# Kernel tuning notes

Hardware: AMD Instinct MI355X
Metric: run time of the kernel (lower is better)

## Reference

```python
import jax, jax.numpy as jnp
import numpy as np

SEQ, D_IN, D_OUT = 8192, 768, 768

def setup_inputs() -> dict:
    key = jax.random.key(0)
    k1, k2, k3, k4 = jax.random.split(key, 4)
    scale = 1.0 / np.sqrt(D_IN)
    return {
        "x": jax.random.normal(k1, (SEQ, D_IN), dtype=jnp.float32),
        "w_q": jax.random.normal(k2, (D_OUT, D_IN), dtype=jnp.float32) * scale,
        "w_k": jax.random.normal(k3, (D_OUT, D_IN), dtype=jnp.float32) * scale,
        "w_v": jax.random.normal(k4, (D_OUT, D_IN), dtype=jnp.float32) * scale,
    }

def reference(x, w_q, w_k, w_v):
    # torch Linear: y = x @ W.T (no bias since qkv_bias=False)
    q = x @ w_q.T  # [S, D]
    k = x @ w_k.T  # [S, D]
    v = x @ w_v.T  # [S, D]
    scores = (q @ k.T) / jnp.sqrt(jnp.asarray(k.shape[-1], x.dtype))  # [S, S]
    attn = jax.nn.softmax(scores, axis=-1)
    return attn @ v  # [S, D]
```

## Files before the change

### kernel.cpp

```cpp
#include <hip/hip_runtime.h>

#define SEQ 8192
#define DIM 768

typedef __attribute__((ext_vector_type(8))) short s16x8;
typedef __attribute__((ext_vector_type(4))) float f32x4;

__device__ __forceinline__ unsigned short f2bf(float f) {
  union { float f; unsigned u; } v; v.f = f;
  unsigned r = v.u + 0x7FFFu + ((v.u >> 16) & 1u);
  return (unsigned short)(r >> 16);
}

__device__ __forceinline__ float bf2f(unsigned short s) {
  union { unsigned u; float f; } v; v.u = ((unsigned)s) << 16;
  return v.f;
}

__device__ __forceinline__ void gll16(const void* gsrc, void* ldst) {
  __builtin_amdgcn_global_load_lds(
      (__attribute__((address_space(1))) unsigned int*)gsrc,
      (__attribute__((address_space(3))) unsigned int*)ldst, 16, 0, 0);
}

#define XN4 (SEQ * DIM / 4)
#define WN4 (DIM * DIM / 4)

__global__ void cast_all_kernel(const float* __restrict__ x, const float* __restrict__ wq,
                                const float* __restrict__ wk, const float* __restrict__ wv,
                                unsigned short* __restrict__ dx, unsigned short* __restrict__ dq,
                                unsigned short* __restrict__ dk, unsigned short* __restrict__ dv) {
  int i = blockIdx.x * blockDim.x + threadIdx.x;
  const float* s;
  unsigned short* d;
  int off;
  if (i < XN4) {
    s = x; d = dx; off = i;
  } else {
    int j = i - XN4;
    int wi = j / WN4;
    off = j - wi * WN4;
    s = (wi == 0) ? wq : ((wi == 1) ? wk : wv);
    d = (wi == 0) ? dq : ((wi == 1) ? dk : dv);
  }
  float4 v = ((const float4*)s)[off];
  ushort4 r; r.x = f2bf(v.x); r.y = f2bf(v.y); r.z = f2bf(v.z); r.w = f2bf(v.w);
  ((ushort4*)d)[off] = r;
}

__global__ __launch_bounds__(256, 2)
void proj_kernel(const unsigned short* __restrict__ X,
                 const unsigned short* __restrict__ Wq,
                 const unsigned short* __restrict__ Wk,
                 const unsigned short* __restrict__ Wv,
                 unsigned short* __restrict__ Qb,
                 unsigned short* __restrict__ Kb,
                 unsigned short* __restrict__ Vtb) {
  __shared__ __align__(16) char lds[65536];
  const int tid = threadIdx.x;
  const int lane = tid & 63, wv = tid >> 6;
  const int l15 = lane & 15, l4 = lane >> 4;
  const int mt = blockIdx.x, nt = blockIdx.y, z = blockIdx.z;
  const unsigned short* W = (z == 0) ? Wq : ((z == 1) ? Wk : Wv);

  f32x4 acc[4][4];
#pragma unroll
  for (int i = 0; i < 4; ++i)
#pragma unroll
    for (int j = 0; j < 4; ++j) acc[i][j] = f32x4{0.f, 0.f, 0.f, 0.f};

  auto stage = [&](int kk) {
    char* At = lds + (kk & 1) * 32768;
    char* Bt = At + 16384;
    const int d0 = kk * 64;
#pragma unroll
    for (int i = 0; i < 4; ++i) {
      int s = i * 256 + tid;
      int row = s >> 3, c = (s & 7) ^ (row & 7);
      gll16(X + (long)(mt * 128 + row) * DIM + d0 + c * 8, At + i * 4096 + (wv << 10));
      gll16(W + (long)(nt * 128 + row) * DIM + d0 + c * 8, Bt + i * 4096 + (wv << 10));
    }
  };

  stage(0);
#pragma unroll 1
  for (int kk = 0; kk < 12; ++kk) {
    __syncthreads();
    if (kk + 1 < 12) stage(kk + 1);
    const char* At = lds + (kk & 1) * 32768;
    const char* Bt = At + 16384;
#pragma unroll
    for (int ks = 0; ks < 2; ++ks) {
      const int c = ks * 4 + l4;
      s16x8 a[4], b[4];
#pragma unroll
      for (int mi = 0; mi < 4; ++mi) {
        int row = (wv & 1) * 64 + mi * 16 + l15;
        a[mi] = *(const s16x8*)(At + row * 128 + ((c ^ (row & 7)) << 4));
      }
#pragma unroll
      for (int ni = 0; ni < 4; ++ni) {
        int row = (wv >> 1) * 64 + ni * 16 + l15;
        b[ni] = *(const s16x8*)(Bt + row * 128 + ((c ^ (row & 7)) << 4));
      }
#pragma unroll
      for (int mi = 0; mi < 4; ++mi)
#pragma unroll
        for (int ni = 0; ni < 4; ++ni)
          acc[mi][ni] = __builtin_amdgcn_mfma_f32_16x16x32_bf16(a[mi], b[ni], acc[mi][ni], 0, 0, 0);
    }
  }

#pragma unroll
  for (int mi = 0; mi < 4; ++mi)
#pragma unroll
    for (int ni = 0; ni < 4; ++ni) {
      int row0 = mt * 128 + (wv & 1) * 64 + mi * 16 + l4 * 4;
      int col = nt * 128 + (wv >> 1) * 64 + ni * 16 + l15;
      if (z == 2) {
        ushort4 r;
        r.x = f2bf(acc[mi][ni][0]); r.y = f2bf(acc[mi][ni][1]);
        r.z = f2bf(acc[mi][ni][2]); r.w = f2bf(acc[mi][ni][3]);
        *(ushort4*)(Vtb + (long)(row0 >> 5) * (DIM * 32) + col * 32 + (row0 & 31)) = r;
      } else {
        unsigned short* dst = (z == 0) ? Qb : Kb;
#pragma unroll
        for (int g = 0; g < 4; ++g)
          dst[(long)(row0 + g) * DIM + col] = f2bf(acc[mi][ni][g]);
      }
    }
}

#define SCALE_LOG2E 0.05205878f

__global__ __launch_bounds__(512, 2)
void flash_kernel(const unsigned short* __restrict__ Q,
                  const unsigned short* __restrict__ K,
                  const unsigned short* __restrict__ V,
                  unsigned short* __restrict__ partp,
                  float* __restrict__ outf,
                  float* __restrict__ lout,
                  int kv_len, int norm_out) {
  __shared__ __align__(16) char lds[131072];
  char* Pl = lds + 98304;
  float* l_part = (float*)lds;

  const int tid = threadIdx.x;
  const int lane = tid & 63, wv = tid >> 6;
  const int l15 = lane & 15, l4 = lane >> 4;
  const int qtile = blockIdx.x, split = blockIdx.y;
  const long kv0 = (long)split * kv_len;
  const long qrow0 = (long)qtile * 64;
  const int R = wv & 1;
  const int C = wv >> 1;

  f32x4 acc_o[4][6];
  float acc_lp[8];
#pragma unroll
  for (int i = 0; i < 4; ++i)
#pragma unroll
    for (int j = 0; j < 6; ++j) acc_o[i][j] = f32x4{0.f, 0.f, 0.f, 0.f};
#pragma unroll
  for (int i = 0; i < 8; ++i) acc_lp[i] = 0.f;

  const int niter = kv_len >> 8;

  auto vchunk = [&](int par, int j) -> char* {
    int base = par ? ((j < 5) ? 40960 + j * 8192 : 90112)
                   : ((j < 5) ? j * 8192 : 81920);
    return lds + base;
  };

  auto stageQK = [&](int r, long kbase) {
    char* Qc = lds + (r & 1) * 40960;
    char* Kc = Qc + 8192;
    const int d0 = r * 64;
    {
      int s = tid;
      int row = s >> 3, c = (s & 7) ^ (row & 7);
      gll16(Q + (qrow0 + row) * DIM + d0 + c * 8, Qc + (wv << 10));
    }
#pragma unroll
    for (int i = 0; i < 4; ++i) {
      int s = i * 512 + tid;
      int row = s >> 3, c = (s & 7) ^ (row & 7);
      gll16(K + (kbase + row) * DIM + d0 + c * 8, Kc + i * 8192 + (wv << 10));
    }
  };

  auto stagePV = [&](int v, long kblk0) {
    const int par = v & 1;
    const long blkbase = (kblk0 + v) * (long)(DIM * 32);
    int s = wv * 64 + lane;
    int rp = s >> 3, p3 = s & 7;
    int orig = p3 ^ (rp & 7);
    int vr_in = rp * 2 + (orig >> 2);
    int k4 = orig & 3;
#pragma unroll
    for (int i = 0; i < 6; ++i)
      gll16(V + blkbase + (long)(i * 128 + vr_in) * 32 + k4 * 8, vchunk(par, i) + (wv << 10));
  };

  stageQK(0, kv0);
#pragma unroll 1
  for (int it = 0; it < niter; ++it) {
    const long kb = kv0 + (long)it * 256;
    const long kblk0 = kb >> 5;

    f32x4 acc_s[2][4];
#pragma unroll
    for (int a = 0; a < 2; ++a)
#pragma unroll
      for (int b = 0; b < 4; ++b) acc_s[a][b] = f32x4{0.f, 0.f, 0.f, 0.f};

#pragma unroll 1
    for (int r = 0; r < 12; ++r) {
      __syncthreads();
      if (r + 1 < 12) stageQK(r + 1, kb);
      else stagePV(0, kblk0);
      const char* Qc = lds + (r & 1) * 40960;
      const char* Kc = Qc + 8192;
#pragma unroll
      for (int ks = 0; ks < 2; ++ks) {
        const int c = ks * 4 + l4;
        s16x8 af[2], bk[4];
#pragma unroll
        for (int rt = 0; rt < 2; ++rt) {
          int row = R * 32 + rt * 16 + l15;
          af[rt] = *(const s16x8*)(Qc + row * 128 + ((c ^ (row & 7)) << 4));
        }
#pragma unroll
        for (int ct = 0; ct < 4; ++ct) {
          int kr = C * 64 + ct * 16 + l15;
          bk[ct] = *(const s16x8*)(Kc + kr * 128 + ((c ^ (kr & 7)) << 4));
        }
#pragma unroll
        for (int rt = 0; rt < 2; ++rt)
#pragma unroll
          for (int ct = 0; ct < 4; ++ct)
            acc_s[rt][ct] = __builtin_amdgcn_mfma_f32_16x16x32_bf16(af[rt], bk[ct], acc_s[rt][ct], 0, 0, 0);
      }
    }

#pragma unroll
    for (int rt = 0; rt < 2; ++rt)
#pragma unroll
      for (int ct = 0; ct < 4; ++ct)
#pragma unroll
        for (int g = 0; g < 4; ++g) {
          float p = exp2f(acc_s[rt][ct][g] * SCALE_LOG2E);
          acc_lp[rt * 4 + g] += p;
          int row = R * 32 + rt * 16 + l4 * 4 + g;
          int col = C * 64 + ct * 16 + l15;
          int off = row * 512 + ((((col >> 3) ^ (row & 7))) << 4) + ((col & 7) << 1);
          *(unsigned short*)(Pl + off) = f2bf(p);
        }

#pragma unroll 1
    for (int v = 0; v < 8; ++v) {
      __syncthreads();
      if (v + 1 < 8) stagePV(v + 1, kblk0);
      else if (it + 1 < niter) stageQK(0, kb + 256);
      const int par = v & 1;
      s16x8 pa[4];
      const int ck = v * 4 + l4;
#pragma unroll
      for (int rs = 0; rs < 4; ++rs) {
        int row = rs * 16 + l15;
        int pc = (ck & ~7) | ((ck & 7) ^ (row & 7));
        pa[rs] = *(const s16x8*)(Pl + row * 512 + (pc << 4));
      }
      const int vr_l = wv * 16 + l15;
      const int rp = vr_l >> 1;
      const int p3 = (((l15 & 1) << 2) | l4) ^ (rp & 7);
#pragma unroll
      for (int cc = 0; cc < 3; ++cc)
#pragma unroll
        for (int t = 0; t < 2; ++t) {
          const char* vcb = vchunk(par, cc * 2 + t);
          s16x8 vb = *(const s16x8*)(vcb + rp * 128 + (p3 << 4));
#pragma unroll
          for (int rs = 0; rs < 4; ++rs)
            acc_o[rs][cc * 2 + t] =
                __builtin_amdgcn_mfma_f32_16x16x32_bf16(pa[rs], vb, acc_o[rs][cc * 2 + t], 0, 0, 0);
        }
    }
  }

#pragma unroll
  for (int i = 0; i < 8; ++i) {
    float v = acc_lp[i];
    v += __shfl_xor(v, 1); v += __shfl_xor(v, 2);
    v += __shfl_xor(v, 4); v += __shfl_xor(v, 8);
    acc_lp[i] = v;
  }
  __syncthreads();
  if (l15 == 0) {
#pragma unroll
    for (int rt = 0; rt < 2; ++rt)
#pragma unroll
      for (int g = 0; g < 4; ++g)
        l_part[C * 64 + R * 32 + rt * 16 + l4 * 4 + g] = acc_lp[rt * 4 + g];
  }
  __syncthreads();

  if (!norm_out) {
    if (tid < 64)
      lout[(long)split * SEQ + qrow0 + tid] =
          l_part[tid] + l_part[64 + tid] + l_part[128 + tid] + l_part[192 + tid];
#pragma unroll
    for (int rt = 0; rt < 4; ++rt) {
      int row = rt * 16 + l4 * 4;
#pragma unroll
      for (int j = 0; j < 6; ++j) {
        int cc = j >> 1, t = j & 1;
        int col = (cc * 16 + wv + 8 * t) * 16 + l15;
#pragma unroll
        for (int g = 0; g < 4; ++g)
          partp[(long)split * SEQ * DIM + (qrow0 + row + g) * DIM + col] = f2bf(acc_o[rt][j][g]);
      }
    }
  } else {
    float linv[4][4];
#pragma unroll
    for (int rt = 0; rt < 4; ++rt)
#pragma unroll
      for (int g = 0; g < 4; ++g) {
        int row = rt * 16 + l4 * 4 + g;
        linv[rt][g] = 1.0f / (l_part[row] + l_part[64 + row] + l_part[128 + row] + l_part[192 + row]);
      }
#pragma unroll
    for (int rt = 0; rt < 4; ++rt) {
      int row = rt * 16 + l4 * 4;
#pragma unroll
      for (int j = 0; j < 6; ++j) {
        int cc = j >> 1, t = j & 1;
        int col = (cc * 16 + wv + 8 * t) * 16 + l15;
#pragma unroll
        for (int g = 0; g < 4; ++g)
          outf[(qrow0 + row + g) * DIM + col] = acc_o[rt][j][g] * linv[rt][g];
      }
    }
  }
}

__global__ void combine_kernel(const unsigned short* __restrict__ part,
                               const float* __restrict__ lsum,
                               float* __restrict__ out, int n4) {
  int i = blockIdx.x * blockDim.x + threadIdx.x;
  if (i >= n4) return;
  int row = (i * 4) / DIM;
  ushort4 p0 = ((const ushort4*)part)[i];
  ushort4 p1 = ((const ushort4*)(part + (long)SEQ * DIM))[i];
  float inv = 1.0f / (lsum[row] + lsum[SEQ + row]);
  float4 o;
  o.x = (bf2f(p0.x) + bf2f(p1.x)) * inv;
  o.y = (bf2f(p0.y) + bf2f(p1.y)) * inv;
  o.z = (bf2f(p0.z) + bf2f(p1.z)) * inv;
  o.w = (bf2f(p0.w) + bf2f(p1.w)) * inv;
  ((float4*)out)[i] = o;
}

extern "C" void kernel_launch(void* const* d_in, const int* in_sizes, int n_in,
                              void* d_out, int out_size, void* d_ws, size_t ws_size,
                              hipStream_t stream) {
  const float* x = (const float*)d_in[0];
  const float* wq = (const float*)d_in[1];
  const float* wk = (const float*)d_in[2];
  const float* wv = (const float*)d_in[3];
  float* out = (float*)d_out;
  char* ws = (char*)d_ws;

  const size_t o_xbf = 0;
  const size_t o_wq = o_xbf + (size_t)SEQ * DIM * 2;
  const size_t o_wk = o_wq + (size_t)DIM * DIM * 2;
  const size_t o_wv = o_wk + (size_t)DIM * DIM * 2;
  const size_t o_q = o_wv + (size_t)DIM * DIM * 2;
  const size_t o_k = o_q + (size_t)SEQ * DIM * 2;
  const size_t o_vt = o_k + (size_t)SEQ * DIM * 2;
  const size_t o_part = o_vt + (size_t)SEQ * DIM * 2;
  const size_t o_l = o_part + (size_t)2 * SEQ * DIM * 2;
  const size_t total_g2 = o_l + (size_t)2 * SEQ * 4;

  unsigned short* Xbf = (unsigned short*)(ws + o_xbf);
  unsigned short* Wqb = (unsigned short*)(ws + o_wq);
  unsigned short* Wkb = (unsigned short*)(ws + o_wk);
  unsigned short* Wvb = (unsigned short*)(ws + o_wv);
  unsigned short* Qb = (unsigned short*)(ws + o_q);
  unsigned short* Kb = (unsigned short*)(ws + o_k);
  unsigned short* Vtb = (unsigned short*)(ws + o_vt);
  unsigned short* part = (unsigned short*)(ws + o_part);
  float* lbuf = (float*)(ws + o_l);

  const int G = (ws_size >= total_g2) ? 2 : 1;

  cast_all_kernel<<<7872, 256, 0, stream>>>(x, wq, wk, wv, Xbf, Wqb, Wkb, Wvb);
  proj_kernel<<<dim3(64, 6, 3), 256, 0, stream>>>(Xbf, Wqb, Wkb, Wvb, Qb, Kb, Vtb);
  if (G == 2) {
    flash_kernel<<<dim3(128, 2), 512, 0, stream>>>(Qb, Kb, Vtb, part, nullptr, lbuf, SEQ / 2, 0);
    combine_kernel<<<6144, 256, 0, stream>>>(part, lbuf, out, SEQ * DIM / 4);
  } else {
    flash_kernel<<<dim3(128, 1), 512, 0, stream>>>(Qb, Kb, Vtb, nullptr, out, nullptr, SEQ, 1);
  }
}
```

Measured before the change: 316.4 us.

## Shrink flash kernel LDS staging and split KV four ways

The flash kernel's LDS staging is halved: Q/K chunks now cover 32 columns instead of 64 over 24 steps, and each V block is staged in two half-D pieces over 16 steps. The footprint drops from 128KB to 80KB, with a new 4-way XOR swizzle for 64-byte rows. The launcher now prefers a 4-way KV split when the workspace allows, and the combine kernel takes a generic split count. The aim is more resident blocks and more grid parallelism, at the cost of twice as many barriers and smaller per-step MFMA batches.

After: 399.6 us. 1.26x slower.

```diff
diff --git a/kernel.cpp b/kernel.cpp
--- a/kernel.cpp
+++ b/kernel.cpp
@@ -141,8 +141,8 @@
                   float* __restrict__ outf,
                   float* __restrict__ lout,
                   int kv_len, int norm_out) {
-  __shared__ __align__(16) char lds[131072];
-  char* Pl = lds + 98304;
+  __shared__ __align__(16) char lds[81920];
+  char* Pl = lds + 49152;
   float* l_part = (float*)lds;
 
   const int tid = threadIdx.x;
@@ -165,40 +165,36 @@
 
   const int niter = kv_len >> 8;
 
-  auto vchunk = [&](int par, int j) -> char* {
-    int base = par ? ((j < 5) ? 40960 + j * 8192 : 90112)
-                   : ((j < 5) ? j * 8192 : 81920);
-    return lds + base;
+  auto stageQK = [&](int r, long kbase) {
+    char* buf = lds + (r & 1) * 24576;
+    char* Qc = buf;
+    char* Kc = buf + 4096;
+    const int d0 = r * 32;
+    if (tid < 256) {
+      int row = tid >> 2, p = tid & 3;
+      int c = p ^ ((row >> 1) & 3);
+      gll16(Q + (qrow0 + row) * DIM + d0 + c * 8, Qc + (wv << 10));
+    }
+#pragma unroll
+    for (int i = 0; i < 2; ++i) {
+      int s = i * 512 + tid;
+      int row = s >> 2, p = s & 3;
+      int c = p ^ ((row >> 1) & 3);
+      gll16(K + (kbase + row) * DIM + d0 + c * 8, Kc + i * 8192 + (wv << 10));
+    }
   };
 
-  auto stageQK = [&](int r, long kbase) {
-    char* Qc = lds + (r & 1) * 40960;
-    char* Kc = Qc + 8192;
-    const int d0 = r * 64;
-    {
-      int s = tid;
-      int row = s >> 3, c = (s & 7) ^ (row & 7);
-      gll16(Q + (qrow0 + row) * DIM + d0 + c * 8, Qc + (wv << 10));
-    }
-#pragma unroll
-    for (int i = 0; i < 4; ++i) {
+  auto stagePV = [&](int v, long kblk0) {
+    char* Vc = lds + (v & 1) * 24576;
+    const long blkbase = (kblk0 + (v >> 1)) * (long)(DIM * 32);
+    const int dh = v & 1;
+#pragma unroll
+    for (int i = 0; i < 3; ++i) {
       int s = i * 512 + tid;
-      int row = s >> 3, c = (s & 7) ^ (row & 7);
-      gll16(K + (kbase + row) * DIM + d0 + c * 8, Kc + i * 8192 + (wv << 10));
-    }
-  };
-
-  auto stagePV = [&](int v, long kblk0) {
-    const int par = v & 1;
-    const long blkbase = (kblk0 + v) * (long)(DIM * 32);
-    int s = wv * 64 + lane;
-    int rp = s >> 3, p3 = s & 7;
-    int orig = p3 ^ (rp & 7);
-    int vr_in = rp * 2 + (orig >> 2);
-    int k4 = orig & 3;
-#pragma unroll
-    for (int i = 0; i < 6; ++i)
-      gll16(V + blkbase + (long)(i * 128 + vr_in) * 32 + k4 * 8, vchunk(par, i) + (wv << 10));
+      int vr = s >> 2, p = s & 3;
+      int c = p ^ ((vr >> 1) & 3);
+      gll16(V + blkbase + (long)(dh * 384 + vr) * 32 + c * 8, Vc + i * 8192 + (wv << 10));
+    }
   };
 
   stageQK(0, kv0);
@@ -214,32 +210,29 @@
       for (int b = 0; b < 4; ++b) acc_s[a][b] = f32x4{0.f, 0.f, 0.f, 0.f};
 
 #pragma unroll 1
-    for (int r = 0; r < 12; ++r) {
+    for (int r = 0; r < 24; ++r) {
       __syncthreads();
-      if (r + 1 < 12) stageQK(r + 1, kb);
+      if (r + 1 < 24) stageQK(r + 1, kb);
       else stagePV(0, kblk0);
-      const char* Qc = lds + (r & 1) * 40960;
-      const char* Kc = Qc + 8192;
-#pragma unroll
-      for (int ks = 0; ks < 2; ++ks) {
-        const int c = ks * 4 + l4;
-        s16x8 af[2], bk[4];
-#pragma unroll
-        for (int rt = 0; rt < 2; ++rt) {
-          int row = R * 32 + rt * 16 + l15;
-          af[rt] = *(const s16x8*)(Qc + row * 128 + ((c ^ (row & 7)) << 4));
-        }
-#pragma unroll
-        for (int ct = 0; ct < 4; ++ct) {
-          int kr = C * 64 + ct * 16 + l15;
-          bk[ct] = *(const s16x8*)(Kc + kr * 128 + ((c ^ (kr & 7)) << 4));
-        }
-#pragma unroll
-        for (int rt = 0; rt < 2; ++rt)
-#pragma unroll
-          for (int ct = 0; ct < 4; ++ct)
-            acc_s[rt][ct] = __builtin_amdgcn_mfma_f32_16x16x32_bf16(af[rt], bk[ct], acc_s[rt][ct], 0, 0, 0);
-      }
+      const char* buf = lds + (r & 1) * 24576;
+      const char* Qc = buf;
+      const char* Kc = buf + 4096;
+      s16x8 af[2], bk[4];
+#pragma unroll
+      for (int rt = 0; rt < 2; ++rt) {
+        int row = R * 32 + rt * 16 + l15;
+        af[rt] = *(const s16x8*)(Qc + row * 64 + ((l4 ^ ((row >> 1) & 3)) << 4));
+      }
+#pragma unroll
+      for (int ct = 0; ct < 4; ++ct) {
+        int kr = C * 64 + ct * 16 + l15;
+        bk[ct] = *(const s16x8*)(Kc + kr * 64 + ((l4 ^ ((kr >> 1) & 3)) << 4));
+      }
+#pragma unroll
+      for (int rt = 0; rt < 2; ++rt)
+#pragma unroll
+        for (int ct = 0; ct < 4; ++ct)
+          acc_s[rt][ct] = __builtin_amdgcn_mfma_f32_16x16x32_bf16(af[rt], bk[ct], acc_s[rt][ct], 0, 0, 0);
     }
 
 #pragma unroll
@@ -256,34 +249,32 @@
           *(unsigned short*)(Pl + off) = f2bf(p);
         }
 
-#pragma unroll 1
-    for (int v = 0; v < 8; ++v) {
+    s16x8 pa[4];
+#pragma unroll 2
+    for (int v = 0; v < 16; ++v) {
       __syncthreads();
-      if (v + 1 < 8) stagePV(v + 1, kblk0);
+      if (v + 1 < 16) stagePV(v + 1, kblk0);
       else if (it + 1 < niter) stageQK(0, kb + 256);
-      const int par = v & 1;
-      s16x8 pa[4];
-      const int ck = v * 4 + l4;
-#pragma unroll
-      for (int rs = 0; rs < 4; ++rs) {
-        int row = rs * 16 + l15;
-        int pc = (ck & ~7) | ((ck & 7) ^ (row & 7));
-        pa[rs] = *(const s16x8*)(Pl + row * 512 + (pc << 4));
-      }
-      const int vr_l = wv * 16 + l15;
-      const int rp = vr_l >> 1;
-      const int p3 = (((l15 & 1) << 2) | l4) ^ (rp & 7);
-#pragma unroll
-      for (int cc = 0; cc < 3; ++cc)
-#pragma unroll
-        for (int t = 0; t < 2; ++t) {
-          const char* vcb = vchunk(par, cc * 2 + t);
-          s16x8 vb = *(const s16x8*)(vcb + rp * 128 + (p3 << 4));
-#pragma unroll
-          for (int rs = 0; rs < 4; ++rs)
-            acc_o[rs][cc * 2 + t] =
-                __builtin_amdgcn_mfma_f32_16x16x32_bf16(pa[rs], vb, acc_o[rs][cc * 2 + t], 0, 0, 0);
+      const char* Vc = lds + (v & 1) * 24576;
+      const int dh = v & 1;
+      if (dh == 0) {
+        const int ck = (v >> 1) * 4 + l4;
+#pragma unroll
+        for (int rs = 0; rs < 4; ++rs) {
+          int row = rs * 16 + l15;
+          int pc = (ck & ~7) | ((ck & 7) ^ (row & 7));
+          pa[rs] = *(const s16x8*)(Pl + row * 512 + (pc << 4));
         }
+      }
+#pragma unroll
+      for (int j = 0; j < 3; ++j) {
+        int vr = j * 128 + wv * 16 + l15;
+        s16x8 vb = *(const s16x8*)(Vc + vr * 64 + ((l4 ^ ((vr >> 1) & 3)) << 4));
+#pragma unroll
+        for (int rs = 0; rs < 4; ++rs)
+          acc_o[rs][dh * 3 + j] =
+              __builtin_amdgcn_mfma_f32_16x16x32_bf16(pa[rs], vb, acc_o[rs][dh * 3 + j], 0, 0, 0);
+      }
     }
   }
 
@@ -346,18 +337,20 @@
 
 __global__ void combine_kernel(const unsigned short* __restrict__ part,
                                const float* __restrict__ lsum,
-                               float* __restrict__ out, int n4) {
+                               float* __restrict__ out, int n4, int nsplit) {
   int i = blockIdx.x * blockDim.x + threadIdx.x;
   if (i >= n4) return;
   int row = (i * 4) / DIM;
-  ushort4 p0 = ((const ushort4*)part)[i];
-  ushort4 p1 = ((const ushort4*)(part + (long)SEQ * DIM))[i];
-  float inv = 1.0f / (lsum[row] + lsum[SEQ + row]);
-  float4 o;
-  o.x = (bf2f(p0.x) + bf2f(p1.x)) * inv;
-  o.y = (bf2f(p0.y) + bf2f(p1.y)) * inv;
-  o.z = (bf2f(p0.z) + bf2f(p1.z)) * inv;
-  o.w = (bf2f(p0.w) + bf2f(p1.w)) * inv;
+  float4 o = {0.f, 0.f, 0.f, 0.f};
+  float l = 0.f;
+#pragma unroll 4
+  for (int g = 0; g < nsplit; ++g) {
+    ushort4 p = ((const ushort4*)(part + (long)g * SEQ * DIM))[i];
+    o.x += bf2f(p.x); o.y += bf2f(p.y); o.z += bf2f(p.z); o.w += bf2f(p.w);
+    l += lsum[(long)g * SEQ + row];
+  }
+  float inv = 1.0f / l;
+  o.x *= inv; o.y *= inv; o.z *= inv; o.w *= inv;
   ((float4*)out)[i] = o;
 }
 
@@ -379,8 +372,10 @@
   const size_t o_k = o_q + (size_t)SEQ * DIM * 2;
   const size_t o_vt = o_k + (size_t)SEQ * DIM * 2;
   const size_t o_part = o_vt + (size_t)SEQ * DIM * 2;
-  const size_t o_l = o_part + (size_t)2 * SEQ * DIM * 2;
-  const size_t total_g2 = o_l + (size_t)2 * SEQ * 4;
+  const size_t o_l4 = o_part + (size_t)4 * SEQ * DIM * 2;
+  const size_t total_g4 = o_l4 + (size_t)4 * SEQ * 4;
+  const size_t o_l2 = o_part + (size_t)2 * SEQ * DIM * 2;
+  const size_t total_g2 = o_l2 + (size_t)2 * SEQ * 4;
 
   unsigned short* Xbf = (unsigned short*)(ws + o_xbf);
   unsigned short* Wqb = (unsigned short*)(ws + o_wq);
@@ -390,15 +385,19 @@
   unsigned short* Kb = (unsigned short*)(ws + o_k);
   unsigned short* Vtb = (unsigned short*)(ws + o_vt);
   unsigned short* part = (unsigned short*)(ws + o_part);
+
+  int G;
+  size_t o_l;
+  if (ws_size >= total_g4) { G = 4; o_l = o_l4; }
+  else if (ws_size >= total_g2) { G = 2; o_l = o_l2; }
+  else { G = 1; o_l = o_part; }
   float* lbuf = (float*)(ws + o_l);
-
-  const int G = (ws_size >= total_g2) ? 2 : 1;
 
   cast_all_kernel<<<7872, 256, 0, stream>>>(x, wq, wk, wv, Xbf, Wqb, Wkb, Wvb);
   proj_kernel<<<dim3(64, 6, 3), 256, 0, stream>>>(Xbf, Wqb, Wkb, Wvb, Qb, Kb, Vtb);
-  if (G == 2) {
-    flash_kernel<<<dim3(128, 2), 512, 0, stream>>>(Qb, Kb, Vtb, part, nullptr, lbuf, SEQ / 2, 0);
-    combine_kernel<<<6144, 256, 0, stream>>>(part, lbuf, out, SEQ * DIM / 4);
+  if (G > 1) {
+    flash_kernel<<<dim3(128, G), 512, 0, stream>>>(Qb, Kb, Vtb, part, nullptr, lbuf, SEQ / G, 0);
+    combine_kernel<<<6144, 256, 0, stream>>>(part, lbuf, out, SEQ * DIM / 4, G);
   } else {
     flash_kernel<<<dim3(128, 1), 512, 0, stream>>>(Qb, Kb, Vtb, nullptr, out, nullptr, SEQ, 1);
   }
```

## Split key range four ways, prefetch P fragments, and raise MFMA wave priority

Applied to the files above, without the earlier changes.

Splits the key dimension into up to four partitions when the workspace is large enough, launching 512 flash blocks instead of 256 and generalising the combine kernel to sum any number of partial outputs. The PV loop is unrolled with double-buffered P fragments so the LDS reads for the next chunk are issued while the current chunk's MFMAs run. s_setprio is raised around the MFMA sequences. The extra split adds partial-output writes and combine traffic, and fixed work per block is amortised over fewer keys.

New measurement: 465.2 us. 47.0% more time.

```diff
diff --git a/kernel.cpp b/kernel.cpp
--- a/kernel.cpp
+++ b/kernel.cpp
@@ -234,11 +234,13 @@
           int kr = C * 64 + ct * 16 + l15;
           bk[ct] = *(const s16x8*)(Kc + kr * 128 + ((c ^ (kr & 7)) << 4));
         }
+        __builtin_amdgcn_s_setprio(1);
 #pragma unroll
         for (int rt = 0; rt < 2; ++rt)
 #pragma unroll
           for (int ct = 0; ct < 4; ++ct)
             acc_s[rt][ct] = __builtin_amdgcn_mfma_f32_16x16x32_bf16(af[rt], bk[ct], acc_s[rt][ct], 0, 0, 0);
+        __builtin_amdgcn_s_setprio(0);
       }
     }
 
@@ -256,20 +258,22 @@
           *(unsigned short*)(Pl + off) = f2bf(p);
         }
 
-#pragma unroll 1
-    for (int v = 0; v < 8; ++v) {
+    s16x8 paA[4], paB[4];
+    auto ldp = [&](s16x8 (&pp)[4], int v) {
+      const int ck = v * 4 + l4;
+#pragma unroll
+      for (int rs = 0; rs < 4; ++rs) {
+        int row = rs * 16 + l15;
+        int pc = (ck & ~7) | ((ck & 7) ^ (row & 7));
+        pp[rs] = *(const s16x8*)(Pl + row * 512 + (pc << 4));
+      }
+    };
+    auto pvchunk = [&](s16x8 (&pa)[4], s16x8 (&pn)[4], int v, bool first) {
       __syncthreads();
       if (v + 1 < 8) stagePV(v + 1, kblk0);
       else if (it + 1 < niter) stageQK(0, kb + 256);
+      if (first) ldp(pa, 0);
       const int par = v & 1;
-      s16x8 pa[4];
-      const int ck = v * 4 + l4;
-#pragma unroll
-      for (int rs = 0; rs < 4; ++rs) {
-        int row = rs * 16 + l15;
-        int pc = (ck & ~7) | ((ck & 7) ^ (row & 7));
-        pa[rs] = *(const s16x8*)(Pl + row * 512 + (pc << 4));
-      }
       const int vr_l = wv * 16 + l15;
       const int rp = vr_l >> 1;
       const int p3 = (((l15 & 1) << 2) | l4) ^ (rp & 7);
@@ -279,12 +283,23 @@
         for (int t = 0; t < 2; ++t) {
           const char* vcb = vchunk(par, cc * 2 + t);
           s16x8 vb = *(const s16x8*)(vcb + rp * 128 + (p3 << 4));
+          __builtin_amdgcn_s_setprio(1);
 #pragma unroll
           for (int rs = 0; rs < 4; ++rs)
             acc_o[rs][cc * 2 + t] =
                 __builtin_amdgcn_mfma_f32_16x16x32_bf16(pa[rs], vb, acc_o[rs][cc * 2 + t], 0, 0, 0);
+          __builtin_amdgcn_s_setprio(0);
         }
-    }
+      if (v + 1 < 8) ldp(pn, v + 1);
+    };
+    pvchunk(paA, paB, 0, true);
+    pvchunk(paB, paA, 1, false);
+    pvchunk(paA, paB, 2, false);
+    pvchunk(paB, paA, 3, false);
+    pvchunk(paA, paB, 4, false);
+    pvchunk(paB, paA, 5, false);
+    pvchunk(paA, paB, 6, false);
+    pvchunk(paB, paA, 7, false);
   }
 
 #pragma unroll
@@ -346,18 +361,20 @@
 
 __global__ void combine_kernel(const unsigned short* __restrict__ part,
                                const float* __restrict__ lsum,
-                               float* __restrict__ out, int n4) {
+                               float* __restrict__ out, int n4, int nsplit) {
   int i = blockIdx.x * blockDim.x + threadIdx.x;
   if (i >= n4) return;
   int row = (i * 4) / DIM;
-  ushort4 p0 = ((const ushort4*)part)[i];
-  ushort4 p1 = ((const ushort4*)(part + (long)SEQ * DIM))[i];
-  float inv = 1.0f / (lsum[row] + lsum[SEQ + row]);
-  float4 o;
-  o.x = (bf2f(p0.x) + bf2f(p1.x)) * inv;
-  o.y = (bf2f(p0.y) + bf2f(p1.y)) * inv;
-  o.z = (bf2f(p0.z) + bf2f(p1.z)) * inv;
-  o.w = (bf2f(p0.w) + bf2f(p1.w)) * inv;
+  float4 o = {0.f, 0.f, 0.f, 0.f};
+  float l = 0.f;
+#pragma unroll 4
+  for (int g = 0; g < nsplit; ++g) {
+    ushort4 p = ((const ushort4*)(part + (long)g * SEQ * DIM))[i];
+    o.x += bf2f(p.x); o.y += bf2f(p.y); o.z += bf2f(p.z); o.w += bf2f(p.w);
+    l += lsum[(long)g * SEQ + row];
+  }
+  float inv = 1.0f / l;
+  o.x *= inv; o.y *= inv; o.z *= inv; o.w *= inv;
   ((float4*)out)[i] = o;
 }
 
@@ -379,8 +396,10 @@
   const size_t o_k = o_q + (size_t)SEQ * DIM * 2;
   const size_t o_vt = o_k + (size_t)SEQ * DIM * 2;
   const size_t o_part = o_vt + (size_t)SEQ * DIM * 2;
-  const size_t o_l = o_part + (size_t)2 * SEQ * DIM * 2;
-  const size_t total_g2 = o_l + (size_t)2 * SEQ * 4;
+  const size_t o_l4 = o_part + (size_t)4 * SEQ * DIM * 2;
+  const size_t total_g4 = o_l4 + (size_t)4 * SEQ * 4;
+  const size_t o_l2 = o_part + (size_t)2 * SEQ * DIM * 2;
+  const size_t total_g2 = o_l2 + (size_t)2 * SEQ * 4;
 
   unsigned short* Xbf = (unsigned short*)(ws + o_xbf);
   unsigned short* Wqb = (unsigned short*)(ws + o_wq);
@@ -390,15 +409,19 @@
   unsigned short* Kb = (unsigned short*)(ws + o_k);
   unsigned short* Vtb = (unsigned short*)(ws + o_vt);
   unsigned short* part = (unsigned short*)(ws + o_part);
+
+  int G;
+  size_t o_l;
+  if (ws_size >= total_g4) { G = 4; o_l = o_l4; }
+  else if (ws_size >= total_g2) { G = 2; o_l = o_l2; }
+  else { G = 1; o_l = o_part; }
   float* lbuf = (float*)(ws + o_l);
-
-  const int G = (ws_size >= total_g2) ? 2 : 1;
 
   cast_all_kernel<<<7872, 256, 0, stream>>>(x, wq, wk, wv, Xbf, Wqb, Wkb, Wvb);
   proj_kernel<<<dim3(64, 6, 3), 256, 0, stream>>>(Xbf, Wqb, Wkb, Wvb, Qb, Kb, Vtb);
-  if (G == 2) {
-    flash_kernel<<<dim3(128, 2), 512, 0, stream>>>(Qb, Kb, Vtb, part, nullptr, lbuf, SEQ / 2, 0);
-    combine_kernel<<<6144, 256, 0, stream>>>(part, lbuf, out, SEQ * DIM / 4);
+  if (G > 1) {
+    flash_kernel<<<dim3(128, G), 512, 0, stream>>>(Qb, Kb, Vtb, part, nullptr, lbuf, SEQ / G, 0);
+    combine_kernel<<<6144, 256, 0, stream>>>(part, lbuf, out, SEQ * DIM / 4, G);
   } else {
     flash_kernel<<<dim3(128, 1), 512, 0, stream>>>(Qb, Kb, Vtb, nullptr, out, nullptr, SEQ, 1);
   }
```
